# Kernel tuning notes

Hardware: AMD Instinct MI355X
Metric: run time of the kernel (lower is better)

## Reference

```python
import jax, jax.numpy as jnp
import numpy as np

B, N, C, H, M = 2, 32768, 256, 8, 64
D = C // H  # 32
EPS = 1e-5


def layernorm(x, g, b):
    mu = x.mean(-1, keepdims=True)
    var = ((x - mu) ** 2).mean(-1, keepdims=True)
    return (x - mu) * jax.lax.rsqrt(var + EPS) * g + b


def setup_inputs() -> dict:
    key = jax.random.key(0)
    ks = jax.random.split(key, 12)
    def w(k, shape, fan_in):
        return jax.random.normal(k, shape, jnp.float32) / np.sqrt(fan_in)
    return {
        "x": jax.random.normal(ks[0], (B, N, C), jnp.float32),
        "ln1_g": jnp.ones((C,), jnp.float32),
        "ln1_b": jnp.zeros((C,), jnp.float32),
        "Wfx": w(ks[1], (C, C), C), "bfx": jnp.zeros((C,), jnp.float32),
        "Wx": w(ks[2], (C, C), C), "bx": jnp.zeros((C,), jnp.float32),
        "Wsl": w(ks[3], (D, M), D), "bsl": jnp.zeros((M,), jnp.float32),
        "temp": jnp.full((1, H, 1, 1), 0.5, jnp.float32),
        "Wq": w(ks[4], (D, D), D),
        "Wk": w(ks[5], (D, D), D),
        "Wv": w(ks[6], (D, D), D),
        "Wo": w(ks[7], (C, C), C), "bo": jnp.zeros((C,), jnp.float32),
        "ln2_g": jnp.ones((C,), jnp.float32),
        "ln2_b": jnp.zeros((C,), jnp.float32),
        "W1": w(ks[8], (C, 4 * C), C), "b1": jnp.zeros((4 * C,), jnp.float32),
        "W2": w(ks[9], (4 * C, C), 4 * C), "b2": jnp.zeros((C,), jnp.float32),
    }


def reference(x, ln1_g, ln1_b, Wfx, bfx, Wx, bx, Wsl, bsl, temp,
              Wq, Wk, Wv, Wo, bo, ln2_g, ln2_b, W1, b1, W2, b2):
    scale = D ** -0.5
    h = layernorm(x, ln1_g, ln1_b)
    # projections -> (B,H,N,D)
    fx_mid = (h @ Wfx + bfx).reshape(B, N, H, D).transpose(0, 2, 1, 3)
    x_mid = (h @ Wx + bx).reshape(B, N, H, D).transpose(0, 2, 1, 3)
    # slice routing: (B,H,N,M)
    logits = (x_mid @ Wsl + bsl) / jnp.clip(temp, 0.1, None)
    sw = jax.nn.softmax(logits, axis=-1)
    slice_norm = jnp.clip(sw.sum(axis=2), 1e-5, None)  # (B,H,M)
    slice_token = jnp.einsum('bhnd,bhnm->bhmd', fx_mid, sw) / slice_norm[..., None]
    # small attention over M slices
    q = slice_token @ Wq
    k = slice_token @ Wk
    v = slice_token @ Wv
    attn = jax.nn.softmax(jnp.einsum('bhmd,bhgd->bhmg', q, k) * scale, axis=-1)
    out_slice = jnp.einsum('bhmg,bhgd->bhmd', attn, v)
    # scatter back to N tokens
    out = jnp.einsum('bhmd,bhnm->bhnd', out_slice, sw)
    out = out.transpose(0, 2, 1, 3).reshape(B, N, C) @ Wo + bo
    x = x + out
    h2 = layernorm(x, ln2_g, ln2_b)
    ffn = jax.nn.gelu(h2 @ W1 + b1, approximate=False) @ W2 + b2
    return x + ffn
```

## Files before the change

kernel.cpp:

```cpp
#include <hip/hip_runtime.h>
#include <hip/hip_bf16.h>

typedef float f32x4 __attribute__((ext_vector_type(4)));
typedef short bf16x8 __attribute__((ext_vector_type(8)));
typedef short short4v __attribute__((ext_vector_type(4)));

constexpr int kB = 2, kN = 32768, kC = 256, kH = 8, kD = 32, kM = 64;
constexpr int kT = kB * kN;

__device__ __forceinline__ float b2f(short s) {
    unsigned u = ((unsigned)(unsigned short)s) << 16;
    return __builtin_bit_cast(float, u);
}
__device__ __forceinline__ short f2b(float f) {
    __hip_bfloat16 h = __float2bfloat16(f);
    return __builtin_bit_cast(short, h);
}
__device__ __forceinline__ float gelu_fast(float x) {
    float x2 = x * x;
    float g2 = x * (2.3022042f + 0.10295342f * x2);
#if __has_builtin(__builtin_amdgcn_exp2f)
    float em = __builtin_amdgcn_exp2f(-g2);
#else
    float em = exp2f(-g2);
#endif
#if __has_builtin(__builtin_amdgcn_rcpf)
    return x * __builtin_amdgcn_rcpf(1.0f + em);
#else
    return x / (1.0f + em);
#endif
}

#if __has_builtin(__builtin_amdgcn_global_load_lds)
__device__ __forceinline__ void gld16(const void* g, void* l) {
    __builtin_amdgcn_global_load_lds((__attribute__((address_space(1))) void*)g,
                                     (__attribute__((address_space(3))) void*)l, 16, 0, 0);
}
#else
__device__ __forceinline__ void gld16(const void* g, void* l) {
    *(bf16x8*)l = *(const bf16x8*)g;
}
#endif

__global__ __launch_bounds__(256) void prep_wt(const float* __restrict__ W,
                                               short* __restrict__ Wt, int K, int N) {
    __shared__ float t[32][33];
    int k0 = blockIdx.x * 32, n0 = blockIdx.y * 32;
    int tx = threadIdx.x & 31, ty = threadIdx.x >> 5;
#pragma unroll
    for (int r = 0; r < 32; r += 8)
        t[ty + r][tx] = W[(size_t)(k0 + ty + r) * N + n0 + tx];
    __syncthreads();
#pragma unroll
    for (int r = 0; r < 32; r += 8)
        Wt[(size_t)(n0 + ty + r) * K + k0 + tx] = f2b(t[tx][ty + r]);
}

__global__ __launch_bounds__(256) void prep_pack(const short* __restrict__ src,
                                                 short* __restrict__ dst, int K, int KT) {
    int g = blockIdx.x * 256 + threadIdx.x;
    int frag = g >> 6, lane = g & 63;
    int nt = frag / KT, kt = frag - nt * KT;
    const short* s = &src[(size_t)(nt * 16 + (lane & 15)) * K + kt * 32 + (lane >> 4) * 8];
    *(bf16x8*)&dst[(size_t)frag * 512 + lane * 8] = *(const bf16x8*)s;
}

__global__ __launch_bounds__(256) void prep_wxsl(const float* __restrict__ Wx,
                                                 const float* __restrict__ Wsl,
                                                 const float* __restrict__ bx,
                                                 const float* __restrict__ bsl,
                                                 short* __restrict__ wxsl_t,
                                                 float* __restrict__ bxsl) {
    int n = blockIdx.x;
    int h = n >> 6, m = n & 63;
    int c = threadIdx.x;
    float s = 0.f;
#pragma unroll 8
    for (int dd = 0; dd < 32; ++dd)
        s += Wx[(size_t)c * 256 + h * 32 + dd] * Wsl[dd * 64 + m];
    wxsl_t[(size_t)n * 256 + c] = f2b(s);
    if (c == 0) {
        float bs = bsl[m];
        for (int dd = 0; dd < 32; ++dd) bs += bx[h * 32 + dd] * Wsl[dd * 64 + m];
        bxsl[n] = bs;
    }
}

template <bool IN_BF16>
__global__ __launch_bounds__(256) void ln_kernel(const void* __restrict__ xin,
                                                 const float* __restrict__ g,
                                                 const float* __restrict__ bb,
                                                 short* __restrict__ out) {
    int row = blockIdx.x * 4 + (threadIdx.x >> 6);
    int lane = threadIdx.x & 63;
    float v[4];
    if constexpr (IN_BF16) {
        short4v s = *((const short4v*)((const short*)xin + (size_t)row * kC) + lane);
#pragma unroll
        for (int j = 0; j < 4; ++j) v[j] = b2f(s[j]);
    } else {
        f32x4 s = *((const f32x4*)((const float*)xin + (size_t)row * kC) + lane);
#pragma unroll
        for (int j = 0; j < 4; ++j) v[j] = s[j];
    }
    float sum = v[0] + v[1] + v[2] + v[3];
#pragma unroll
    for (int o = 32; o; o >>= 1) sum += __shfl_xor(sum, o);
    float mu = sum * (1.0f / 256.0f);
    float c[4];
    float s2 = 0.f;
#pragma unroll
    for (int j = 0; j < 4; ++j) { c[j] = v[j] - mu; s2 += c[j] * c[j]; }
#pragma unroll
    for (int o = 32; o; o >>= 1) s2 += __shfl_xor(s2, o);
    float inv = rsqrtf(s2 * (1.0f / 256.0f) + 1e-5f);
    f32x4 gv = *((const f32x4*)g + lane);
    f32x4 bv = *((const f32x4*)bb + lane);
    short4v o;
#pragma unroll
    for (int j = 0; j < 4; ++j) o[j] = f2b(c[j] * inv * gv[j] + bv[j]);
    *((short4v*)(out + (size_t)row * kC) + lane) = o;
}

template <int K, int N, int EPI>
__global__ __launch_bounds__(256) void mfma_gemm(const short* __restrict__ A,
                                                 const short* __restrict__ Bt,
                                                 const float* __restrict__ bias,
                                                 const void* __restrict__ res,
                                                 void* __restrict__ Cout) {
    __shared__ __align__(16) short As[128 * 64];
    __shared__ __align__(16) short Bs[128 * 64];
    const int tid = threadIdx.x;
    const int lane = tid & 63;
    const int w = tid >> 6, wr = w >> 1, wc = w & 1;
    const int bm = blockIdx.x * 128, bn = blockIdx.y * 128;
    const int l15 = lane & 15, l16 = lane >> 4;
    f32x4 acc[4][4] = {};
    for (int k0 = 0; k0 < K; k0 += 64) {
        __syncthreads();
#pragma unroll
        for (int l = 0; l < 4; ++l) {
            int li = tid + l * 256;
            int r = li >> 3, s = li & 7;
            int kof = k0 + ((s ^ (r & 7)) << 3);
            gld16(&A[(size_t)(bm + r) * K + kof], &As[li * 8]);
            gld16(&Bt[(size_t)(bn + r) * K + kof], &Bs[li * 8]);
        }
        __syncthreads();
#pragma unroll
        for (int ks = 0; ks < 2; ++ks) {
            bf16x8 av[4], bv[4];
            int q = ks * 4 + l16;
#pragma unroll
            for (int mi = 0; mi < 4; ++mi) {
                int row = wr * 64 + mi * 16 + l15;
                av[mi] = *(const bf16x8*)(&As[row * 64 + ((q ^ (row & 7)) << 3)]);
            }
#pragma unroll
            for (int ni = 0; ni < 4; ++ni) {
                int row = wc * 64 + ni * 16 + l15;
                bv[ni] = *(const bf16x8*)(&Bs[row * 64 + ((q ^ (row & 7)) << 3)]);
            }
#pragma unroll
            for (int mi = 0; mi < 4; ++mi)
#pragma unroll
                for (int ni = 0; ni < 4; ++ni)
                    acc[mi][ni] = __builtin_amdgcn_mfma_f32_16x16x32_bf16(
                        av[mi], bv[ni], acc[mi][ni], 0, 0, 0);
        }
    }
#pragma unroll
    for (int mi = 0; mi < 4; ++mi) {
#pragma unroll
        for (int ni = 0; ni < 4; ++ni) {
            int col = bn + wc * 64 + ni * 16 + l15;
            float bcol = bias[col];
#pragma unroll
            for (int r = 0; r < 4; ++r) {
                size_t row = (size_t)bm + wr * 64 + mi * 16 + l16 * 4 + r;
                float v = acc[mi][ni][r] + bcol;
                size_t off = row * N + col;
                if (EPI == 0) {
                    ((short*)Cout)[off] = f2b(v);
                } else {
                    ((short*)Cout)[off] = f2b(v + ((const float*)res)[off]);
                }
            }
        }
    }
}

__global__ __launch_bounds__(256) void proj_dual(const short* __restrict__ A,
                                                 const short* __restrict__ Bt,
                                                 const float* __restrict__ bfx,
                                                 const float* __restrict__ bxsl,
                                                 short* __restrict__ fxout,
                                                 short* __restrict__ Lout) {
    __shared__ __align__(16) short As[128 * 64];
    __shared__ __align__(16) short Bs[128 * 64];
    const int tid = threadIdx.x;
    const int lane = tid & 63;
    const int w = tid >> 6, wr = w >> 1, wc = w & 1;
    const int bm = blockIdx.x * 128, bn = blockIdx.y * 128;
    const int l15 = lane & 15, l16 = lane >> 4;
    f32x4 acc[4][4] = {};
    for (int k0 = 0; k0 < 256; k0 += 64) {
        __syncthreads();
#pragma unroll
        for (int l = 0; l < 4; ++l) {
            int li = tid + l * 256;
            int r = li >> 3, s = li & 7;
            int kof = k0 + ((s ^ (r & 7)) << 3);
            gld16(&A[(size_t)(bm + r) * 256 + kof], &As[li * 8]);
            gld16(&Bt[(size_t)(bn + r) * 256 + kof], &Bs[li * 8]);
        }
        __syncthreads();
#pragma unroll
        for (int ks = 0; ks < 2; ++ks) {
            bf16x8 av[4], bv[4];
            int q = ks * 4 + l16;
#pragma unroll
            for (int mi = 0; mi < 4; ++mi) {
                int row = wr * 64 + mi * 16 + l15;
                av[mi] = *(const bf16x8*)(&As[row * 64 + ((q ^ (row & 7)) << 3)]);
            }
#pragma unroll
            for (int ni = 0; ni < 4; ++ni) {
                int row = wc * 64 + ni * 16 + l15;
                bv[ni] = *(const bf16x8*)(&Bs[row * 64 + ((q ^ (row & 7)) << 3)]);
            }
#pragma unroll
            for (int mi = 0; mi < 4; ++mi)
#pragma unroll
                for (int ni = 0; ni < 4; ++ni)
                    acc[mi][ni] = __builtin_amdgcn_mfma_f32_16x16x32_bf16(
                        av[mi], bv[ni], acc[mi][ni], 0, 0, 0);
        }
    }
#pragma unroll
    for (int mi = 0; mi < 4; ++mi) {
#pragma unroll
        for (int ni = 0; ni < 4; ++ni) {
            int col = bn + wc * 64 + ni * 16 + l15;
            float bcol = (col < 256) ? bfx[col] : bxsl[col - 256];
#pragma unroll
            for (int r = 0; r < 4; ++r) {
                size_t row = (size_t)bm + wr * 64 + mi * 16 + l16 * 4 + r;
                float v = acc[mi][ni][r] + bcol;
                if (col < 256)
                    fxout[row * 256 + col] = f2b(v);
                else
                    Lout[row * 512 + (col - 256)] = f2b(v);
            }
        }
    }
}

__global__ __launch_bounds__(256, 2) void ffn_fused(const short* __restrict__ h2,
                                                    const short* __restrict__ xres,
                                                    const short* __restrict__ w1p,
                                                    const short* __restrict__ w2p,
                                                    const float* __restrict__ b1,
                                                    const float* __restrict__ b2,
                                                    float* __restrict__ out) {
    __shared__ __align__(16) short As[64 * 256];
    __shared__ __align__(16) short mids[2][64 * 128];
    const int tid = threadIdx.x;
    const int lane = tid & 63, w = tid >> 6;
    const int l15 = lane & 15, l16 = lane >> 4;
    const int bm = blockIdx.x * 64;
#pragma unroll
    for (int l = 0; l < 8; ++l) {
        int li = tid + l * 256;
        int r = li >> 5, s = li & 31;
        gld16(&h2[(size_t)(bm + r) * 256 + ((s ^ (r & 7)) << 3)], &As[li * 8]);
    }
    __syncthreads();
    f32x4 acc2[4][4] = {};
    f32x4 accm[2][4];

#define FFN_GEMM1(jc)                                                                     \
    {                                                                                     \
        _Pragma("unroll") for (int tj = 0; tj < 4; ++tj) {                                \
            accm[0][tj] = f32x4{0.f, 0.f, 0.f, 0.f};                                      \
            accm[1][tj] = f32x4{0.f, 0.f, 0.f, 0.f};                                      \
        }                                                                                 \
        const short* wp0 = &w1p[(size_t)(((jc)*8 + w * 2) * 8) * 512 + lane * 8];         \
        _Pragma("unroll") for (int ks = 0; ks < 8; ++ks) {                                \
            bf16x8 aw0 = *(const bf16x8*)(wp0 + ks * 512);                                \
            bf16x8 aw1 = *(const bf16x8*)(wp0 + (8 + ks) * 512);                          \
            _Pragma("unroll") for (int tj = 0; tj < 4; ++tj) {                            \
                int row = tj * 16 + l15;                                                  \
                int q = ks * 4 + l16;                                                     \
                bf16x8 bh = *(const bf16x8*)&As[row * 256 + ((q ^ (row & 7)) << 3)];      \
                accm[0][tj] =                                                             \
                    __builtin_amdgcn_mfma_f32_16x16x32_bf16(aw0, bh, accm[0][tj], 0, 0, 0); \
                accm[1][tj] =                                                             \
                    __builtin_amdgcn_mfma_f32_16x16x32_bf16(aw1, bh, accm[1][tj], 0, 0, 0); \
            }                                                                             \
        }                                                                                 \
    }

#define FFN_WRITE(jc)                                                                     \
    {                                                                                     \
        _Pragma("unroll") for (int mcf = 0; mcf < 2; ++mcf) {                             \
            int mc0 = w * 32 + mcf * 16 + l16 * 4;                                        \
            f32x4 bc1 = *(const f32x4*)&b1[(jc)*128 + mc0];                               \
            _Pragma("unroll") for (int tj = 0; tj < 4; ++tj) {                            \
                int token = tj * 16 + l15;                                                \
                short4v pk;                                                               \
                _Pragma("unroll") for (int r = 0; r < 4; ++r)                             \
                    pk[r] = f2b(gelu_fast(accm[mcf][tj][r] + bc1[r]));                    \
                *(short4v*)((char*)mids[(jc)&1] + token * 256 +                           \
                            ((mc0 * 2) ^ ((token & 7) << 4))) = pk;                       \
            }                                                                             \
        }                                                                                 \
    }

#define FFN_GEMM2(jc)                                                                     \
    {                                                                                     \
        _Pragma("unroll") for (int ks = 0; ks < 4; ++ks) {                                \
            int q = ks * 4 + l16;                                                         \
            bf16x8 am[4];                                                                 \
            _Pragma("unroll") for (int mi = 0; mi < 4; ++mi) {                            \
                int row = mi * 16 + l15;                                                  \
                am[mi] = *(const bf16x8*)((const char*)mids[(jc)&1] + row * 256 +         \
                                          ((q * 16) ^ ((row & 7) << 4)));                 \
            }                                                                             \
            _Pragma("unroll") for (int ni = 0; ni < 4; ++ni) {                            \
                bf16x8 bv = *(const bf16x8*)&w2p[(size_t)((w * 4 + ni) * 32 + (jc)*4 +    \
                                                          ks) *                           \
                                                     512 +                                \
                                                 lane * 8];                               \
                _Pragma("unroll") for (int mi = 0; mi < 4; ++mi)                          \
                    acc2[mi][ni] = __builtin_amdgcn_mfma_f32_16x16x32_bf16(               \
                        am[mi], bv, acc2[mi][ni], 0, 0, 0);                               \
            }                                                                             \
        }                                                                                 \
    }

    FFN_GEMM1(0);
#pragma unroll
    for (int jc = 0; jc < 8; ++jc) {
        __syncthreads();
        if (jc > 0) FFN_GEMM2(jc - 1);
        FFN_WRITE(jc);
        if (jc < 7) FFN_GEMM1(jc + 1);
    }
    __syncthreads();
    FFN_GEMM2(7);
#undef FFN_GEMM1
#undef FFN_WRITE
#undef FFN_GEMM2

#pragma unroll
    for (int mi = 0; mi < 4; ++mi)
#pragma unroll
        for (int ni = 0; ni < 4; ++ni) {
            int col = w * 64 + ni * 16 + l15;
            float bc2 = b2[col];
#pragma unroll
            for (int r = 0; r < 4; ++r) {
                size_t row = (size_t)bm + mi * 16 + l16 * 4 + r;
                out[row * 256 + col] = acc2[mi][ni][r] + bc2 + b2f(xres[row * 256 + col]);
            }
        }
}

__global__ __launch_bounds__(256) void fused_slice(const short* __restrict__ L,
                                                   const short* __restrict__ fx,
                                                   const float* __restrict__ temp,
                                                   float* __restrict__ stoken,
                                                   float* __restrict__ snorm) {
    int h = blockIdx.y;
    int t0g = blockIdx.x * 2048;
    int b = t0g >> 15;
    int tid = threadIdx.x;
    int lane = tid & 63, w = tid >> 6;
    int l15 = lane & 15, l16 = lane >> 4;
    __shared__ __align__(16) char smem[57344];
    float inv_t = 1.0f / fmaxf(temp[h], 0.1f);
    const int tt2 = tid * 2;
#pragma unroll
    for (int r = 0; r < 16; ++r) {
        int row = 32 + r;
        *(short*)(smem + 32768 + row * 512 + (tt2 ^ ((row & 7) << 4))) =
            (r == 0) ? (short)0x3F80 : (short)0;
    }
    f32x4 acc[4][3] = {};
    const int swz = (l15 & 7) << 4;
    const int abase = l15 * 512;
    for (int sub = 0; sub < 8; ++sub) {
        __syncthreads();
        int t = t0g + sub * 256 + tid;
        float lg[64];
        const short* Lp = &L[(size_t)t * 512 + h * 64];
#pragma unroll
        for (int mv = 0; mv < 8; ++mv) {
            bf16x8 v = *(const bf16x8*)(Lp + mv * 8);
#pragma unroll
            for (int j = 0; j < 8; ++j) lg[mv * 8 + j] = b2f(v[j]) * inv_t;
        }
        float mx = -1e30f;
#pragma unroll
        for (int m = 0; m < 64; ++m) mx = fmaxf(mx, lg[m]);
        float sum = 0.f;
#pragma unroll
        for (int m = 0; m < 64; ++m) { lg[m] = expf(lg[m] - mx); sum += lg[m]; }
        float inv = 1.0f / sum;
#pragma unroll
        for (int m = 0; m < 64; ++m)
            *(short*)(smem + m * 512 + (tt2 ^ ((m & 7) << 4))) = f2b(lg[m] * inv);
        const short* fxp = &fx[(size_t)t * 256 + h * 32];
#pragma unroll
        for (int mv = 0; mv < 4; ++mv) {
            bf16x8 v = *(const bf16x8*)(fxp + mv * 8);
#pragma unroll
            for (int j = 0; j < 8; ++j)
                *(short*)(smem + 32768 + (mv * 8 + j) * 512 + (tt2 ^ (j << 4))) = v[j];
        }
        __syncthreads();
#pragma unroll
        for (int ks = 0; ks < 2; ++ks) {
            int off = ((w * 8 + ks * 4 + l16) * 16) ^ swz;
            bf16x8 a0 = *(const bf16x8*)(smem + abase + off);
            bf16x8 a1 = *(const bf16x8*)(smem + abase + 8192 + off);
            bf16x8 a2 = *(const bf16x8*)(smem + abase + 16384 + off);
            bf16x8 a3 = *(const bf16x8*)(smem + abase + 24576 + off);
            bf16x8 b0 = *(const bf16x8*)(smem + 32768 + abase + off);
            bf16x8 b1 = *(const bf16x8*)(smem + 32768 + abase + 8192 + off);
            bf16x8 b2v = *(const bf16x8*)(smem + 32768 + abase + 16384 + off);
            acc[0][0] = __builtin_amdgcn_mfma_f32_16x16x32_bf16(a0, b0, acc[0][0], 0, 0, 0);
            acc[0][1] = __builtin_amdgcn_mfma_f32_16x16x32_bf16(a0, b1, acc[0][1], 0, 0, 0);
            acc[0][2] = __builtin_amdgcn_mfma_f32_16x16x32_bf16(a0, b2v, acc[0][2], 0, 0, 0);
            acc[1][0] = __builtin_amdgcn_mfma_f32_16x16x32_bf16(a1, b0, acc[1][0], 0, 0, 0);
            acc[1][1] = __builtin_amdgcn_mfma_f32_16x16x32_bf16(a1, b1, acc[1][1], 0, 0, 0);
            acc[1][2] = __builtin_amdgcn_mfma_f32_16x16x32_bf16(a1, b2v, acc[1][2], 0, 0, 0);
            acc[2][0] = __builtin_amdgcn_mfma_f32_16x16x32_bf16(a2, b0, acc[2][0], 0, 0, 0);
            acc[2][1] = __builtin_amdgcn_mfma_f32_16x16x32_bf16(a2, b1, acc[2][1], 0, 0, 0);
            acc[2][2] = __builtin_amdgcn_mfma_f32_16x16x32_bf16(a2, b2v, acc[2][2], 0, 0, 0);
            acc[3][0] = __builtin_amdgcn_mfma_f32_16x16x32_bf16(a3, b0, acc[3][0], 0, 0, 0);
            acc[3][1] = __builtin_amdgcn_mfma_f32_16x16x32_bf16(a3, b1, acc[3][1], 0, 0, 0);
            acc[3][2] = __builtin_amdgcn_mfma_f32_16x16x32_bf16(a3, b2v, acc[3][2], 0, 0, 0);
        }
    }
    __syncthreads();
    float* red = (float*)smem;
#pragma unroll
    for (int mi = 0; mi < 4; ++mi)
#pragma unroll
        for (int ni = 0; ni < 3; ++ni)
#pragma unroll
            for (int r = 0; r < 4; ++r)
                red[w * 3072 + (mi * 16 + l16 * 4 + r) * 48 + ni * 16 + l15] =
                    acc[mi][ni][r];
    __syncthreads();
    for (int e = tid; e < 3072; e += 256) {
        float s = red[e] + red[3072 + e] + red[6144 + e] + red[9216 + e];
        int m = e / 48, n = e - m * 48;
        if (n < 32)
            atomicAdd(&stoken[(size_t)((b * 8 + h) * 64 + m) * 32 + n], s);
        else if (n == 32)
            atomicAdd(&snorm[(b * 8 + h) * 64 + m], s);
    }
}

__global__ __launch_bounds__(256) void slice_attn_kernel(const float* __restrict__ stoken,
                                                         const float* __restrict__ snorm,
                                                         const float* __restrict__ Wq,
                                                         const float* __restrict__ Wk,
                                                         const float* __restrict__ Wv,
                                                         float* __restrict__ oslice) {
    int bh = blockIdx.x;
    int tid = threadIdx.x;
    int m = tid & 63, grp = tid >> 6;
    __shared__ float st_s[64][33];
    __shared__ float q_s[64][33];
    __shared__ float k_s[64][33];
    __shared__ float v_s[64][33];
    __shared__ float w_s[3][32][32];
    __shared__ float sc_s[64][65];
    __shared__ float nrm_s[64];
    for (int i = tid; i < 3072; i += 256) {
        const float* W = (i < 1024) ? Wq : (i < 2048 ? Wk : Wv);
        int r = i & 1023;
        w_s[i >> 10][r >> 5][r & 31] = W[r];
    }
    if (tid < 64) nrm_s[tid] = 1.0f / fmaxf(snorm[bh * 64 + tid], 1e-5f);
    for (int i = tid; i < 512; i += 256) {
        int mm = i >> 3, dq = (i & 7) << 2;
        f32x4 v = *(const f32x4*)&stoken[(size_t)bh * 2048 + mm * 32 + dq];
        *(f32x4*)&st_s[mm][dq] = v;
    }
    __syncthreads();
    {
        int d0 = grp * 8;
        float qr[8] = {}, kr[8] = {}, vr[8] = {};
#pragma unroll
        for (int dd = 0; dd < 32; ++dd) {
            float s = st_s[m][dd];
#pragma unroll
            for (int j = 0; j < 8; ++j) {
                qr[j] += s * w_s[0][dd][d0 + j];
                kr[j] += s * w_s[1][dd][d0 + j];
                vr[j] += s * w_s[2][dd][d0 + j];
            }
        }
        float nm = nrm_s[m];
#pragma unroll
        for (int j = 0; j < 8; ++j) {
            q_s[m][d0 + j] = qr[j] * nm;
            k_s[m][d0 + j] = kr[j] * nm;
            v_s[m][d0 + j] = vr[j] * nm;
        }
    }
    __syncthreads();
    {
#pragma unroll
        for (int gg = 0; gg < 16; ++gg) {
            int g = grp * 16 + gg;
            float s = 0.f;
#pragma unroll
            for (int dd = 0; dd < 32; ++dd) s += q_s[m][dd] * k_s[g][dd];
            sc_s[m][g] = s * 0.17677669529663687f;
        }
    }
    __syncthreads();
    if (tid < 64) {
        float mx = -1e30f;
#pragma unroll
        for (int g = 0; g < 64; ++g) mx = fmaxf(mx, sc_s[tid][g]);
        float sum = 0.f;
#pragma unroll
        for (int g = 0; g < 64; ++g) {
            float e = expf(sc_s[tid][g] - mx);
            sc_s[tid][g] = e;
            sum += e;
        }
        float inv = 1.0f / sum;
#pragma unroll
        for (int g = 0; g < 64; ++g) sc_s[tid][g] *= inv;
    }
    __syncthreads();
    {
        int d0 = grp * 8;
        float o[8] = {};
#pragma unroll
        for (int g = 0; g < 64; ++g) {
            float p = sc_s[m][g];
#pragma unroll
            for (int j = 0; j < 8; ++j) o[j] += p * v_s[g][d0 + j];
        }
#pragma unroll
        for (int j = 0; j < 8; ++j)
            oslice[(size_t)bh * 2048 + m * 32 + d0 + j] = o[j];
    }
}

__global__ __launch_bounds__(256) void scatter_mfma(const short* __restrict__ L,
                                                    const float* __restrict__ oslice,
                                                    const float* __restrict__ temp,
                                                    short* __restrict__ y) {
    int h = blockIdx.y;
    int t0 = blockIdx.x * 256;
    int b = t0 >> 15;
    int tid = threadIdx.x;
    int lane = tid & 63, w = tid >> 6;
    int l15 = lane & 15, l16 = lane >> 4;
    __shared__ __align__(16) char smem[36864];
    float inv_t = 1.0f / fmaxf(temp[h], 0.1f);
    const float* osp = &oslice[(size_t)(b * 8 + h) * 2048];
    for (int i = tid; i < 2048; i += 256) {
        int m = i >> 5, d = i & 31;
        *(short*)(smem + 32768 + d * 128 + ((2 * m) ^ ((d & 7) << 4))) = f2b(osp[m * 32 + d]);
    }
    float lg[64];
    const short* Lp = &L[(size_t)(t0 + tid) * 512 + h * 64];
#pragma unroll
    for (int mv = 0; mv < 8; ++mv) {
        bf16x8 v = *(const bf16x8*)(Lp + mv * 8);
#pragma unroll
        for (int j = 0; j < 8; ++j) lg[mv * 8 + j] = b2f(v[j]) * inv_t;
    }
    float mx = -1e30f;
#pragma unroll
    for (int m = 0; m < 64; ++m) mx = fmaxf(mx, lg[m]);
    float sum = 0.f;
#pragma unroll
    for (int m = 0; m < 64; ++m) { lg[m] = expf(lg[m] - mx); sum += lg[m]; }
    float inv = 1.0f / sum;
    int tswz = (tid & 7) << 4;
#pragma unroll
    for (int jm = 0; jm < 8; ++jm) {
        bf16x8 o;
#pragma unroll
        for (int j = 0; j < 8; ++j) o[j] = f2b(lg[jm * 8 + j] * inv);
        *(bf16x8*)(smem + tid * 128 + ((jm * 16) ^ tswz)) = o;
    }
    __syncthreads();
    const int swz = (l15 & 7) << 4;
    f32x4 acc[4][2] = {};
#pragma unroll
    for (int ks = 0; ks < 2; ++ks) {
        int off = ((ks * 4 + l16) * 16) ^ swz;
        bf16x8 b0 = *(const bf16x8*)(smem + 32768 + l15 * 128 + off);
        bf16x8 b1 = *(const bf16x8*)(smem + 32768 + (16 + l15) * 128 + off);
#pragma unroll
        for (int i = 0; i < 4; ++i) {
            bf16x8 a = *(const bf16x8*)(smem + (w * 64 + i * 16 + l15) * 128 + off);
            acc[i][0] = __builtin_amdgcn_mfma_f32_16x16x32_bf16(a, b0, acc[i][0], 0, 0, 0);
            acc[i][1] = __builtin_amdgcn_mfma_f32_16x16x32_bf16(a, b1, acc[i][1], 0, 0, 0);
        }
    }
#pragma unroll
    for (int i = 0; i < 4; ++i)
#pragma unroll
        for (int ni = 0; ni < 2; ++ni)
#pragma unroll
            for (int r = 0; r < 4; ++r) {
                int tr = w * 64 + i * 16 + l16 * 4 + r;
                y[(size_t)(t0 + tr) * 256 + h * 32 + ni * 16 + l15] = f2b(acc[i][ni][r]);
            }
}

extern "C" void kernel_launch(void* const* d_in, const int* in_sizes, int n_in,
                              void* d_out, int out_size, void* d_ws, size_t ws_size,
                              hipStream_t stream) {
    (void)in_sizes; (void)n_in; (void)out_size; (void)ws_size;
    const float* x    = (const float*)d_in[0];
    const float* ln1g = (const float*)d_in[1];
    const float* ln1b = (const float*)d_in[2];
    const float* Wfx  = (const float*)d_in[3];
    const float* bfx  = (const float*)d_in[4];
    const float* Wx   = (const float*)d_in[5];
    const float* bx   = (const float*)d_in[6];
    const float* Wsl  = (const float*)d_in[7];
    const float* bsl  = (const float*)d_in[8];
    const float* temp = (const float*)d_in[9];
    const float* Wq   = (const float*)d_in[10];
    const float* Wk   = (const float*)d_in[11];
    const float* Wv   = (const float*)d_in[12];
    const float* Wo   = (const float*)d_in[13];
    const float* bo   = (const float*)d_in[14];
    const float* ln2g = (const float*)d_in[15];
    const float* ln2b = (const float*)d_in[16];
    const float* W1   = (const float*)d_in[17];
    const float* b1   = (const float*)d_in[18];
    const float* W2   = (const float*)d_in[19];
    const float* b2   = (const float*)d_in[20];
    float* out = (float*)d_out;

    constexpr size_t SLOT = (size_t)kT * kC * 2;
    char* ws = (char*)d_ws;
    short* S0 = (short*)(ws);
    short* S1 = (short*)(ws + SLOT);
    char*  S3 = ws + 3 * SLOT;
    short* wfx_t  = (short*)(S3);
    short* wxsl_t = (short*)(S3 + 131072);
    short* wo_t   = (short*)(S3 + 393216);
    short* w1_t   = (short*)(S3 + 524288);
    short* w2_t   = (short*)(S3 + 1048576);
    float* bxsl   = (float*)(S3 + 1572864);
    float* stoken = (float*)(S3 + 1574912);
    float* snorm  = (float*)(S3 + 1705984);
    float* oslice = (float*)(S3 + 1710080);
    short* w1p    = (short*)(S3 + 1841152);
    short* w2p    = (short*)(S3 + 2365440);

    short* h    = S0;
    short* fx   = S1;
    short* y    = S0;
    short* xres = S1;
    short* h2   = S0;
    short* Lbuf = (short*)d_out;

    prep_wt<<<dim3(8, 8), 256, 0, stream>>>(Wfx, wfx_t, 256, 256);
    prep_wt<<<dim3(8, 8), 256, 0, stream>>>(Wo, wo_t, 256, 256);
    prep_wt<<<dim3(8, 32), 256, 0, stream>>>(W1, w1_t, 256, 1024);
    prep_wt<<<dim3(32, 8), 256, 0, stream>>>(W2, w2_t, 1024, 256);
    prep_wxsl<<<512, 256, 0, stream>>>(Wx, Wsl, bx, bsl, wxsl_t, bxsl);
    prep_pack<<<128, 256, 0, stream>>>(w1_t, w1p, 256, 8);
    prep_pack<<<128, 256, 0, stream>>>(w2_t, w2p, 1024, 32);
    hipMemsetAsync(stoken, 0, 131072 + 4096, stream);

    ln_kernel<false><<<kT / 4, 256, 0, stream>>>(x, ln1g, ln1b, h);
    proj_dual<<<dim3(kT / 128, 6), 256, 0, stream>>>(h, wfx_t, bfx, bxsl, fx, Lbuf);
    fused_slice<<<dim3(kT / 2048, kH), 256, 0, stream>>>(Lbuf, fx, temp, stoken, snorm);
    slice_attn_kernel<<<kB * kH, 256, 0, stream>>>(stoken, snorm, Wq, Wk, Wv, oslice);
    scatter_mfma<<<dim3(kT / 256, kH), 256, 0, stream>>>(Lbuf, oslice, temp, y);
    mfma_gemm<256, 256, 1><<<dim3(kT / 128, 2), 256, 0, stream>>>(y, wo_t, bo, x, xres);
    ln_kernel<true><<<kT / 4, 256, 0, stream>>>(xres, ln2g, ln2b, h2);
    ffn_fused<<<kT / 64, 256, 0, stream>>>(h2, xres, w1p, w2p, b1, b2, out);
}
```

Baseline: 334.4 us.

## Fuse scatter with Wo projection and fold LayerNorm2 into the FFN kernel

```diff
diff --git a/kernel.cpp b/kernel.cpp
--- a/kernel.cpp
+++ b/kernel.cpp
@@ -122,74 +122,6 @@
     *((short4v*)(out + (size_t)row * kC) + lane) = o;
 }
 
-template <int K, int N, int EPI>
-__global__ __launch_bounds__(256) void mfma_gemm(const short* __restrict__ A,
-                                                 const short* __restrict__ Bt,
-                                                 const float* __restrict__ bias,
-                                                 const void* __restrict__ res,
-                                                 void* __restrict__ Cout) {
-    __shared__ __align__(16) short As[128 * 64];
-    __shared__ __align__(16) short Bs[128 * 64];
-    const int tid = threadIdx.x;
-    const int lane = tid & 63;
-    const int w = tid >> 6, wr = w >> 1, wc = w & 1;
-    const int bm = blockIdx.x * 128, bn = blockIdx.y * 128;
-    const int l15 = lane & 15, l16 = lane >> 4;
-    f32x4 acc[4][4] = {};
-    for (int k0 = 0; k0 < K; k0 += 64) {
-        __syncthreads();
-#pragma unroll
-        for (int l = 0; l < 4; ++l) {
-            int li = tid + l * 256;
-            int r = li >> 3, s = li & 7;
-            int kof = k0 + ((s ^ (r & 7)) << 3);
-            gld16(&A[(size_t)(bm + r) * K + kof], &As[li * 8]);
-            gld16(&Bt[(size_t)(bn + r) * K + kof], &Bs[li * 8]);
-        }
-        __syncthreads();
-#pragma unroll
-        for (int ks = 0; ks < 2; ++ks) {
-            bf16x8 av[4], bv[4];
-            int q = ks * 4 + l16;
-#pragma unroll
-            for (int mi = 0; mi < 4; ++mi) {
-                int row = wr * 64 + mi * 16 + l15;
-                av[mi] = *(const bf16x8*)(&As[row * 64 + ((q ^ (row & 7)) << 3)]);
-            }
-#pragma unroll
-            for (int ni = 0; ni < 4; ++ni) {
-                int row = wc * 64 + ni * 16 + l15;
-                bv[ni] = *(const bf16x8*)(&Bs[row * 64 + ((q ^ (row & 7)) << 3)]);
-            }
-#pragma unroll
-            for (int mi = 0; mi < 4; ++mi)
-#pragma unroll
-                for (int ni = 0; ni < 4; ++ni)
-                    acc[mi][ni] = __builtin_amdgcn_mfma_f32_16x16x32_bf16(
-                        av[mi], bv[ni], acc[mi][ni], 0, 0, 0);
-        }
-    }
-#pragma unroll
-    for (int mi = 0; mi < 4; ++mi) {
-#pragma unroll
-        for (int ni = 0; ni < 4; ++ni) {
-            int col = bn + wc * 64 + ni * 16 + l15;
-            float bcol = bias[col];
-#pragma unroll
-            for (int r = 0; r < 4; ++r) {
-                size_t row = (size_t)bm + wr * 64 + mi * 16 + l16 * 4 + r;
-                float v = acc[mi][ni][r] + bcol;
-                size_t off = row * N + col;
-                if (EPI == 0) {
-                    ((short*)Cout)[off] = f2b(v);
-                } else {
-                    ((short*)Cout)[off] = f2b(v + ((const float*)res)[off]);
-                }
-            }
-        }
-    }
-}
-
 __global__ __launch_bounds__(256) void proj_dual(const short* __restrict__ A,
                                                  const short* __restrict__ Bt,
                                                  const float* __restrict__ bfx,
@@ -256,12 +188,13 @@
     }
 }
 
-__global__ __launch_bounds__(256, 2) void ffn_fused(const short* __restrict__ h2,
-                                                    const short* __restrict__ xres,
+__global__ __launch_bounds__(256, 2) void ffn_fused(const short* __restrict__ xres,
                                                     const short* __restrict__ w1p,
                                                     const short* __restrict__ w2p,
                                                     const float* __restrict__ b1,
                                                     const float* __restrict__ b2,
+                                                    const float* __restrict__ ln2g,
+                                                    const float* __restrict__ ln2b,
                                                     float* __restrict__ out) {
     __shared__ __align__(16) short As[64 * 256];
     __shared__ __align__(16) short mids[2][64 * 128];
@@ -269,11 +202,45 @@
     const int lane = tid & 63, w = tid >> 6;
     const int l15 = lane & 15, l16 = lane >> 4;
     const int bm = blockIdx.x * 64;
-#pragma unroll
-    for (int l = 0; l < 8; ++l) {
-        int li = tid + l * 256;
-        int r = li >> 5, s = li & 31;
-        gld16(&h2[(size_t)(bm + r) * 256 + ((s ^ (r & 7)) << 3)], &As[li * 8]);
+    {
+        int r = tid >> 2, qq = tid & 3;
+        const short* xp = &xres[(size_t)(bm + r) * 256 + qq * 64];
+        bf16x8 xv[8];
+        float sum = 0.f;
+#pragma unroll
+        for (int v = 0; v < 8; ++v) {
+            xv[v] = *(const bf16x8*)(xp + v * 8);
+#pragma unroll
+            for (int j = 0; j < 8; ++j) sum += b2f(xv[v][j]);
+        }
+        sum += __shfl_xor(sum, 1);
+        sum += __shfl_xor(sum, 2);
+        float mu = sum * (1.0f / 256.0f);
+        float sq = 0.f;
+#pragma unroll
+        for (int v = 0; v < 8; ++v)
+#pragma unroll
+            for (int j = 0; j < 8; ++j) {
+                float c = b2f(xv[v][j]) - mu;
+                sq += c * c;
+            }
+        sq += __shfl_xor(sq, 1);
+        sq += __shfl_xor(sq, 2);
+        float inv = rsqrtf(sq * (1.0f / 256.0f) + 1e-5f);
+#pragma unroll
+        for (int v = 0; v < 8; ++v) {
+            f32x4 g0 = *(const f32x4*)&ln2g[qq * 64 + v * 8];
+            f32x4 g1 = *(const f32x4*)&ln2g[qq * 64 + v * 8 + 4];
+            f32x4 bb0 = *(const f32x4*)&ln2b[qq * 64 + v * 8];
+            f32x4 bb1 = *(const f32x4*)&ln2b[qq * 64 + v * 8 + 4];
+            bf16x8 o;
+#pragma unroll
+            for (int j = 0; j < 4; ++j) {
+                o[j] = f2b((b2f(xv[v][j]) - mu) * inv * g0[j] + bb0[j]);
+                o[4 + j] = f2b((b2f(xv[v][4 + j]) - mu) * inv * g1[j] + bb1[j]);
+            }
+            *(bf16x8*)((char*)As + r * 512 + (((qq * 8 + v) * 16) ^ ((r & 7) << 4))) = o;
+        }
     }
     __syncthreads();
     f32x4 acc2[4][4] = {};
@@ -557,70 +524,119 @@
     }
 }
 
-__global__ __launch_bounds__(256) void scatter_mfma(const short* __restrict__ L,
-                                                    const float* __restrict__ oslice,
-                                                    const float* __restrict__ temp,
-                                                    short* __restrict__ y) {
-    int h = blockIdx.y;
-    int t0 = blockIdx.x * 256;
-    int b = t0 >> 15;
-    int tid = threadIdx.x;
-    int lane = tid & 63, w = tid >> 6;
-    int l15 = lane & 15, l16 = lane >> 4;
-    __shared__ __align__(16) char smem[36864];
-    float inv_t = 1.0f / fmaxf(temp[h], 0.1f);
-    const float* osp = &oslice[(size_t)(b * 8 + h) * 2048];
-    for (int i = tid; i < 2048; i += 256) {
-        int m = i >> 5, d = i & 31;
-        *(short*)(smem + 32768 + d * 128 + ((2 * m) ^ ((d & 7) << 4))) = f2b(osp[m * 32 + d]);
-    }
-    float lg[64];
-    const short* Lp = &L[(size_t)(t0 + tid) * 512 + h * 64];
-#pragma unroll
-    for (int mv = 0; mv < 8; ++mv) {
-        bf16x8 v = *(const bf16x8*)(Lp + mv * 8);
-#pragma unroll
-        for (int j = 0; j < 8; ++j) lg[mv * 8 + j] = b2f(v[j]) * inv_t;
-    }
-    float mx = -1e30f;
-#pragma unroll
-    for (int m = 0; m < 64; ++m) mx = fmaxf(mx, lg[m]);
-    float sum = 0.f;
-#pragma unroll
-    for (int m = 0; m < 64; ++m) { lg[m] = expf(lg[m] - mx); sum += lg[m]; }
-    float inv = 1.0f / sum;
-    int tswz = (tid & 7) << 4;
-#pragma unroll
-    for (int jm = 0; jm < 8; ++jm) {
-        bf16x8 o;
-#pragma unroll
-        for (int j = 0; j < 8; ++j) o[j] = f2b(lg[jm * 8 + j] * inv);
-        *(bf16x8*)(smem + tid * 128 + ((jm * 16) ^ tswz)) = o;
-    }
-    __syncthreads();
-    const int swz = (l15 & 7) << 4;
-    f32x4 acc[4][2] = {};
-#pragma unroll
-    for (int ks = 0; ks < 2; ++ks) {
-        int off = ((ks * 4 + l16) * 16) ^ swz;
-        bf16x8 b0 = *(const bf16x8*)(smem + 32768 + l15 * 128 + off);
-        bf16x8 b1 = *(const bf16x8*)(smem + 32768 + (16 + l15) * 128 + off);
-#pragma unroll
-        for (int i = 0; i < 4; ++i) {
-            bf16x8 a = *(const bf16x8*)(smem + (w * 64 + i * 16 + l15) * 128 + off);
-            acc[i][0] = __builtin_amdgcn_mfma_f32_16x16x32_bf16(a, b0, acc[i][0], 0, 0, 0);
-            acc[i][1] = __builtin_amdgcn_mfma_f32_16x16x32_bf16(a, b1, acc[i][1], 0, 0, 0);
-        }
-    }
-#pragma unroll
-    for (int i = 0; i < 4; ++i)
-#pragma unroll
-        for (int ni = 0; ni < 2; ++ni)
+__global__ __launch_bounds__(256) void scatter_wo(const short* __restrict__ L,
+                                                  const float* __restrict__ oslice,
+                                                  const float* __restrict__ temp,
+                                                  const short* __restrict__ wop,
+                                                  const float* __restrict__ bo,
+                                                  const float* __restrict__ x,
+                                                  short* __restrict__ xres) {
+    __shared__ __align__(16) char ys[32768];
+    __shared__ __align__(16) char sw_s[2][8192];
+    __shared__ __align__(16) char os_t[2][4096];
+    const int tid = threadIdx.x;
+    const int lane = tid & 63, w = tid >> 6;
+    const int l15 = lane & 15, l16 = lane >> 4;
+    const int t0 = blockIdx.x * 64;
+    const int bn = blockIdx.y * 128;
+    const int b = t0 >> 15;
+    for (int rnd = 0; rnd < 4; ++rnd) {
+        int h0 = rnd * 2;
+        __syncthreads();
+        if (tid < 128) {
+            int hh = tid >> 6, token = tid & 63;
+            int hsel = h0 + hh;
+            float inv_t = 1.0f / fmaxf(temp[hsel], 0.1f);
+            const short* Lp = &L[(size_t)(t0 + token) * 512 + hsel * 64];
+            float lg[64];
+#pragma unroll
+            for (int mv = 0; mv < 8; ++mv) {
+                bf16x8 v = *(const bf16x8*)(Lp + mv * 8);
+#pragma unroll
+                for (int j = 0; j < 8; ++j) lg[mv * 8 + j] = b2f(v[j]) * inv_t;
+            }
+            float mx = -1e30f;
+#pragma unroll
+            for (int m = 0; m < 64; ++m) mx = fmaxf(mx, lg[m]);
+            float sum = 0.f;
+#pragma unroll
+            for (int m = 0; m < 64; ++m) { lg[m] = expf(lg[m] - mx); sum += lg[m]; }
+            float inv = 1.0f / sum;
+            int tswz = (token & 7) << 4;
+#pragma unroll
+            for (int jm = 0; jm < 8; ++jm) {
+                bf16x8 o;
+#pragma unroll
+                for (int j = 0; j < 8; ++j) o[j] = f2b(lg[jm * 8 + j] * inv);
+                *(bf16x8*)(sw_s[hh] + token * 128 + ((jm * 16) ^ tswz)) = o;
+            }
+        } else {
+            for (int i = tid - 128; i < 4096; i += 128) {
+                int hh = i >> 11, j = i & 2047;
+                int m = j >> 5, d = j & 31;
+                *(short*)(os_t[hh] + d * 128 + ((2 * m) ^ ((d & 7) << 4))) =
+                    f2b(oslice[(size_t)(b * 8 + h0 + hh) * 2048 + j]);
+            }
+        }
+        __syncthreads();
+        int trow = w * 16 + l15;
+        int tswz2 = (trow & 7) << 4;
+#pragma unroll
+        for (int hh = 0; hh < 2; ++hh) {
+            f32x4 acc[2] = {};
+#pragma unroll
+            for (int ks = 0; ks < 2; ++ks) {
+                int off = (ks * 4 + l16) * 16;
+                bf16x8 bt = *(const bf16x8*)(sw_s[hh] + trow * 128 + (off ^ tswz2));
+                bf16x8 a0 = *(const bf16x8*)(os_t[hh] + l15 * 128 + (off ^ ((l15 & 7) << 4)));
+                bf16x8 a1 = *(const bf16x8*)(os_t[hh] + (16 + l15) * 128 +
+                                             (off ^ (((16 + l15) & 7) << 4)));
+                acc[0] = __builtin_amdgcn_mfma_f32_16x16x32_bf16(a0, bt, acc[0], 0, 0, 0);
+                acc[1] = __builtin_amdgcn_mfma_f32_16x16x32_bf16(a1, bt, acc[1], 0, 0, 0);
+            }
+#pragma unroll
+            for (int df = 0; df < 2; ++df) {
+                short4v pk;
+#pragma unroll
+                for (int r = 0; r < 4; ++r) pk[r] = f2b(acc[df][r]);
+                *(short4v*)(ys + (size_t)trow * 512 +
+                            (((h0 + hh) * 64 + df * 32 + l16 * 8) ^ tswz2)) = pk;
+            }
+        }
+    }
+    __syncthreads();
+    f32x4 acc2[4][2] = {};
+#pragma unroll
+    for (int kt = 0; kt < 8; ++kt) {
+        bf16x8 av[4];
+#pragma unroll
+        for (int tf = 0; tf < 4; ++tf) {
+            int row = tf * 16 + l15;
+            av[tf] = *(const bf16x8*)(ys + row * 512 +
+                                      ((kt * 64 + l16 * 16) ^ ((row & 7) << 4)));
+        }
+#pragma unroll
+        for (int nf = 0; nf < 2; ++nf) {
+            int nt = blockIdx.y * 8 + w * 2 + nf;
+            bf16x8 bv = *(const bf16x8*)&wop[(size_t)(nt * 8 + kt) * 512 + lane * 8];
+#pragma unroll
+            for (int tf = 0; tf < 4; ++tf)
+                acc2[tf][nf] = __builtin_amdgcn_mfma_f32_16x16x32_bf16(av[tf], bv,
+                                                                       acc2[tf][nf], 0, 0, 0);
+        }
+    }
+#pragma unroll
+    for (int tf = 0; tf < 4; ++tf)
+#pragma unroll
+        for (int nf = 0; nf < 2; ++nf) {
+            int col = bn + w * 32 + nf * 16 + l15;
+            float bc = bo[col];
 #pragma unroll
             for (int r = 0; r < 4; ++r) {
-                int tr = w * 64 + i * 16 + l16 * 4 + r;
-                y[(size_t)(t0 + tr) * 256 + h * 32 + ni * 16 + l15] = f2b(acc[i][ni][r]);
-            }
+                size_t row = (size_t)t0 + tf * 16 + l16 * 4 + r;
+                xres[row * 256 + col] = f2b(acc2[tf][nf][r] + bc + x[row * 256 + col]);
+            }
+        }
 }
 
 extern "C" void kernel_launch(void* const* d_in, const int* in_sizes, int n_in,
@@ -666,12 +682,11 @@
     float* oslice = (float*)(S3 + 1710080);
     short* w1p    = (short*)(S3 + 1841152);
     short* w2p    = (short*)(S3 + 2365440);
+    short* wop    = (short*)(S3 + 2889728);
 
     short* h    = S0;
     short* fx   = S1;
-    short* y    = S0;
     short* xres = S1;
-    short* h2   = S0;
     short* Lbuf = (short*)d_out;
 
     prep_wt<<<dim3(8, 8), 256, 0, stream>>>(Wfx, wfx_t, 256, 256);
@@ -681,14 +696,13 @@
     prep_wxsl<<<512, 256, 0, stream>>>(Wx, Wsl, bx, bsl, wxsl_t, bxsl);
     prep_pack<<<128, 256, 0, stream>>>(w1_t, w1p, 256, 8);
     prep_pack<<<128, 256, 0, stream>>>(w2_t, w2p, 1024, 32);
+    prep_pack<<<32, 256, 0, stream>>>(wo_t, wop, 256, 8);
     hipMemsetAsync(stoken, 0, 131072 + 4096, stream);
 
     ln_kernel<false><<<kT / 4, 256, 0, stream>>>(x, ln1g, ln1b, h);
     proj_dual<<<dim3(kT / 128, 6), 256, 0, stream>>>(h, wfx_t, bfx, bxsl, fx, Lbuf);
     fused_slice<<<dim3(kT / 2048, kH), 256, 0, stream>>>(Lbuf, fx, temp, stoken, snorm);
     slice_attn_kernel<<<kB * kH, 256, 0, stream>>>(stoken, snorm, Wq, Wk, Wv, oslice);
-    scatter_mfma<<<dim3(kT / 256, kH), 256, 0, stream>>>(Lbuf, oslice, temp, y);
-    mfma_gemm<256, 256, 1><<<dim3(kT / 128, 2), 256, 0, stream>>>(y, wo_t, bo, x, xres);
-    ln_kernel<true><<<kT / 4, 256, 0, stream>>>(xres, ln2g, ln2b, h2);
-    ffn_fused<<<kT / 64, 256, 0, stream>>>(h2, xres, w1p, w2p, b1, b2, out);
-}
+    scatter_wo<<<dim3(kT / 64, 2), 256, 0, stream>>>(Lbuf, oslice, temp, wop, bo, x, xres);
+    ffn_fused<<<kT / 64, 256, 0, stream>>>(xres, w1p, w2p, b1, b2, ln2g, ln2b, out);
+}
```

After: 351.4 us. 1.05x slower.

## Replace tiled projection GEMM with packed-weight row-block kernel reading B from global

Applied to the files above, without the earlier changes.

```diff
diff --git a/kernel.cpp b/kernel.cpp
--- a/kernel.cpp
+++ b/kernel.cpp
@@ -190,68 +190,65 @@
     }
 }
 
-__global__ __launch_bounds__(256) void proj_dual(const short* __restrict__ A,
-                                                 const short* __restrict__ Bt,
-                                                 const float* __restrict__ bfx,
-                                                 const float* __restrict__ bxsl,
-                                                 short* __restrict__ fxout,
-                                                 short* __restrict__ Lout) {
-    __shared__ __align__(16) short As[128 * 64];
-    __shared__ __align__(16) short Bs[128 * 64];
+__global__ __launch_bounds__(256, 3) void proj_packed(const short* __restrict__ h,
+                                                      const short* __restrict__ wp,
+                                                      const float* __restrict__ bfx,
+                                                      const float* __restrict__ bxsl,
+                                                      short* __restrict__ fxout,
+                                                      short* __restrict__ Lout) {
+    __shared__ __align__(16) short As[64 * 256];
     const int tid = threadIdx.x;
-    const int lane = tid & 63;
-    const int w = tid >> 6, wr = w >> 1, wc = w & 1;
-    const int bm = blockIdx.x * 128, bn = blockIdx.y * 128;
+    const int lane = tid & 63, w = tid >> 6;
     const int l15 = lane & 15, l16 = lane >> 4;
-    f32x4 acc[4][4] = {};
-    for (int k0 = 0; k0 < 256; k0 += 64) {
-        __syncthreads();
-#pragma unroll
-        for (int l = 0; l < 4; ++l) {
-            int li = tid + l * 256;
-            int r = li >> 3, s = li & 7;
-            int kof = k0 + ((s ^ (r & 7)) << 3);
-            gld16(&A[(size_t)(bm + r) * 256 + kof], &As[li * 8]);
-            gld16(&Bt[(size_t)(bn + r) * 256 + kof], &Bs[li * 8]);
-        }
-        __syncthreads();
-#pragma unroll
-        for (int ks = 0; ks < 2; ++ks) {
-            bf16x8 av[4], bv[4];
-            int q = ks * 4 + l16;
-#pragma unroll
-            for (int mi = 0; mi < 4; ++mi) {
-                int row = wr * 64 + mi * 16 + l15;
-                av[mi] = *(const bf16x8*)(&As[row * 64 + ((q ^ (row & 7)) << 3)]);
-            }
-#pragma unroll
-            for (int ni = 0; ni < 4; ++ni) {
-                int row = wc * 64 + ni * 16 + l15;
-                bv[ni] = *(const bf16x8*)(&Bs[row * 64 + ((q ^ (row & 7)) << 3)]);
-            }
-#pragma unroll
-            for (int mi = 0; mi < 4; ++mi)
-#pragma unroll
-                for (int ni = 0; ni < 4; ++ni)
-                    acc[mi][ni] = __builtin_amdgcn_mfma_f32_16x16x32_bf16(
-                        av[mi], bv[ni], acc[mi][ni], 0, 0, 0);
-        }
-    }
-#pragma unroll
-    for (int mi = 0; mi < 4; ++mi) {
-#pragma unroll
-        for (int ni = 0; ni < 4; ++ni) {
-            int col = bn + wc * 64 + ni * 16 + l15;
-            float bcol = (col < 256) ? bfx[col] : bxsl[col - 256];
-#pragma unroll
-            for (int r = 0; r < 4; ++r) {
-                size_t row = (size_t)bm + wr * 64 + mi * 16 + l16 * 4 + r;
-                float v = acc[mi][ni][r] + bcol;
-                if (col < 256)
-                    fxout[row * 256 + col] = f2b(v);
-                else
-                    Lout[row * 512 + (col - 256)] = f2b(v);
-            }
+    const int bm = blockIdx.x * 64;
+#pragma unroll
+    for (int l = 0; l < 8; ++l) {
+        int li = tid + l * 256;
+        int r = li >> 5, s = li & 31;
+        gld16(&h[(size_t)(bm + r) * 256 + ((s ^ (r & 7)) << 3)], &As[li * 8]);
+    }
+    __syncthreads();
+#pragma unroll
+    for (int pass = 0; pass < 2; ++pass) {
+        f32x4 acc[4][6];
+#pragma unroll
+        for (int tj = 0; tj < 4; ++tj)
+#pragma unroll
+            for (int cf = 0; cf < 6; ++cf) acc[tj][cf] = f32x4{0.f, 0.f, 0.f, 0.f};
+        int cfbase = pass * 24 + w * 6;
+#pragma unroll
+        for (int kf = 0; kf < 8; ++kf) {
+            bf16x8 av[4];
+#pragma unroll
+            for (int tj = 0; tj < 4; ++tj) {
+                int row = tj * 16 + l15;
+                av[tj] = *(const bf16x8*)&As[row * 256 + (((kf * 4 + l16) ^ (row & 7)) << 3)];
+            }
+#pragma unroll
+            for (int cf = 0; cf < 6; ++cf) {
+                bf16x8 bv =
+                    *(const bf16x8*)&wp[(size_t)((cfbase + cf) * 8 + kf) * 512 + lane * 8];
+#pragma unroll
+                for (int tj = 0; tj < 4; ++tj)
+                    acc[tj][cf] = __builtin_amdgcn_mfma_f32_16x16x32_bf16(av[tj], bv,
+                                                                          acc[tj][cf], 0, 0, 0);
+            }
+        }
+#pragma unroll
+        for (int cf = 0; cf < 6; ++cf) {
+            int col = (cfbase + cf) * 16 + l15;
+            float bc = (col < 256) ? bfx[col] : bxsl[col - 256];
+#pragma unroll
+            for (int tj = 0; tj < 4; ++tj)
+#pragma unroll
+                for (int r = 0; r < 4; ++r) {
+                    size_t row = (size_t)bm + tj * 16 + l16 * 4 + r;
+                    float v = acc[tj][cf][r] + bc;
+                    if (col < 256)
+                        fxout[row * 256 + col] = f2b(v);
+                    else
+                        Lout[row * 512 + (col - 256)] = f2b(v);
+                }
         }
     }
 }
@@ -655,17 +652,18 @@
     short* S0 = (short*)(ws);
     short* S1 = (short*)(ws + SLOT);
     char*  S3 = ws + 3 * SLOT;
-    short* wfx_t  = (short*)(S3);
-    short* wxsl_t = (short*)(S3 + 131072);
-    short* wo_t   = (short*)(S3 + 393216);
-    short* w1_t   = (short*)(S3 + 524288);
-    short* w2_t   = (short*)(S3 + 1048576);
-    float* bxsl   = (float*)(S3 + 1572864);
-    float* stoken = (float*)(S3 + 1574912);
-    float* snorm  = (float*)(S3 + 1705984);
-    float* oslice = (float*)(S3 + 1710080);
-    short* w1p    = (short*)(S3 + 1841152);
-    short* w2p    = (short*)(S3 + 2365440);
+    short* wfx_t   = (short*)(S3);
+    short* wxsl_t  = (short*)(S3 + 131072);
+    short* wo_t    = (short*)(S3 + 393216);
+    short* w1_t    = (short*)(S3 + 524288);
+    short* w2_t    = (short*)(S3 + 1048576);
+    float* bxsl    = (float*)(S3 + 1572864);
+    float* stoken  = (float*)(S3 + 1574912);
+    float* snorm   = (float*)(S3 + 1705984);
+    float* oslice  = (float*)(S3 + 1710080);
+    short* w1p     = (short*)(S3 + 1841152);
+    short* w2p     = (short*)(S3 + 2365440);
+    short* wfxsl_p = (short*)(S3 + 2889728);
 
     short* h    = S0;
     short* fx   = S1;
@@ -681,10 +679,11 @@
     prep_wxsl<<<512, 256, 0, stream>>>(Wx, Wsl, bx, bsl, wxsl_t, bxsl);
     prep_pack<<<128, 256, 0, stream>>>(w1_t, w1p, 256, 8);
     prep_pack<<<128, 256, 0, stream>>>(w2_t, w2p, 1024, 32);
+    prep_pack<<<96, 256, 0, stream>>>(wfx_t, wfxsl_p, 256, 8);
     hipMemsetAsync(stoken, 0, 131072 + 4096, stream);
 
     ln_kernel<false><<<kT / 4, 256, 0, stream>>>(x, ln1g, ln1b, h);
-    proj_dual<<<dim3(kT / 128, 6), 256, 0, stream>>>(h, wfx_t, bfx, bxsl, fx, Lbuf);
+    proj_packed<<<kT / 64, 256, 0, stream>>>(h, wfxsl_p, bfx, bxsl, fx, Lbuf);
     fused_slice<<<dim3(kT / 2048, kH), 256, 0, stream>>>(Lbuf, fx, temp, stoken, snorm);
     slice_attn_kernel<<<kB * kH, 256, 0, stream>>>(stoken, snorm, Wq, Wk, Wv, oslice);
     scatter_mfma<<<dim3(kT / 256, kH), 256, 0, stream>>>(Lbuf, oslice, temp, y);
```

After: 396.2 us. 18.5% more time.
